# Kernel tuning notes

Measured on AMD Instinct MI355X. Metric: run time of the kernel, lower is better.

The kernel has to match this reference:

```python
import jax, jax.numpy as jnp
import numpy as np

B, T, DM, H = 1, 1024, 1024, 16
D = DM // H
RANK = 32
CONV = 3


def setup_inputs() -> dict:
    key = jax.random.key(0)
    ks = jax.random.split(key, 9)
    s = lambda k, shape, sc: jax.random.normal(k, shape, dtype=jnp.float32) * sc
    return {
        "x": s(ks[0], (B, T, DM), 1.0),
        "Wq": s(ks[1], (DM, DM), DM ** -0.5),
        "Wk": s(ks[2], (DM, DM), DM ** -0.5),
        "Wv": s(ks[3], (DM, DM), DM ** -0.5),
        "Ww1": s(ks[4], (DM, RANK), DM ** -0.5),
        "Ww2": s(ks[5], (RANK, DM), RANK ** -0.5),
        "conv_w": s(ks[6], (DM, CONV), CONV ** -0.5),
        "Wb": s(ks[7], (DM, H), DM ** -0.5),
        "Wo": s(ks[8], (DM, DM), DM ** -0.5),
    }


def _short_conv_silu(x, conv_w):
    # causal depthwise conv1d (torch semantics, kernel size CONV, no bias) + SiLU
    # y[t] = sum_m conv_w[:, m] * x[t - (CONV-1) + m]
    tl = x.shape[1]
    x_pad = jnp.pad(x, ((0, 0), (CONV - 1, 0), (0, 0)))
    y = sum(conv_w[:, m] * x_pad[:, m:m + tl, :] for m in range(CONV))
    return jax.nn.silu(y)


def _path_forward(x, Wq, Wk, Wv, Ww1, Ww2, conv_w, Wb, Wo):
    # projections
    q = (x @ Wq).reshape(B, T, H, D)
    k = (x @ Wk).reshape(B, T, H, D)
    v = (x @ Wv).reshape(B, T, H, D)
    # low-rank w projection -> causal short conv + silu -> per-head l2 norm
    w = _short_conv_silu((x @ Ww1) @ Ww2, conv_w).reshape(B, T, H, D)
    w = w * jax.lax.rsqrt(jnp.sum(w * w, axis=-1, keepdims=True) + 1e-6)
    beta = 2.0 * jax.nn.sigmoid(x @ Wb)  # [B,T,H], beta in (0,2)

    # -> [B,H,T,D] / [B,H,T]
    q, k, v, w = (jnp.transpose(a, (0, 2, 1, 3)) for a in (q, k, v, w))
    beta = jnp.transpose(beta, (0, 2, 1))

    # PaTH scores: S[i,j] = q_i^T prod_{s=j+1..i} (I - beta_s w_s w_s^T) k_j, i >= j.
    # Exact parallel (UT-transform) form:
    #   G[i,j] = q_i.w_j - sum_{j<s<=i} G[i,s] * beta_s (w_s.w_j)
    #   => G @ (I + M) = tril(Q W^T),  M[s,j] = beta_s (w_s.w_j) for s>j (strict lower)
    #   S = Q K^T - G @ Mk,            Mk[s,j] = beta_s (w_s.k_j) for s>j (strict lower)
    idx = jnp.arange(T)
    strict = idx[:, None] > idx[None, :]
    causal = idx[:, None] >= idx[None, :]

    bw = beta[..., None] * w  # [B,H,T,D]
    M = jnp.where(strict, jnp.einsum('bhsd,bhjd->bhsj', bw, w), 0.0)
    A = jnp.eye(T, dtype=x.dtype) + M  # unit lower triangular
    Aqw = jnp.where(causal, jnp.einsum('bhid,bhsd->bhis', q, w), 0.0)
    G = jax.lax.linalg.triangular_solve(A, Aqw, left_side=False, lower=True,
                                        unit_diagonal=True)
    Mk = jnp.where(strict, jnp.einsum('bhsd,bhjd->bhsj', bw, k), 0.0)
    S = jnp.einsum('bhid,bhjd->bhij', q, k) - jnp.einsum('bhis,bhsj->bhij', G, Mk)
    S = jnp.where(causal, S * (D ** -0.5), -jnp.inf)
    P = jax.nn.softmax(S, axis=-1)
    o = jnp.einsum('bhij,bhjd->bhid', P, v)
    o = jnp.transpose(o, (0, 2, 1, 3)).reshape(B, T, DM)
    return o @ Wo


def reference(x, Wq, Wk, Wv, Ww1, Ww2, conv_w, Wb, Wo):
    return _path_forward(x, Wq, Wk, Wv, Ww1, Ww2, conv_w, Wb, Wo)
```

## Files before the change

### kernel.cpp

```cpp
#include <hip/hip_runtime.h>
#include <math.h>

#define TSEQ 1024
#define DMODEL 1024
#define NH 16
#define HD 64
#define RANK 32

typedef __attribute__((ext_vector_type(8))) short bf16x8;
typedef __attribute__((ext_vector_type(4))) float f32x4;

__device__ __forceinline__ unsigned short f2b(float f) {
    unsigned int u = __float_as_uint(f);
    u += 0x7fffu + ((u >> 16) & 1u);
    return (unsigned short)(u >> 16);
}
__device__ __forceinline__ float b2f(unsigned short h) {
    return __uint_as_float(((unsigned int)h) << 16);
}
__device__ __forceinline__ void split2(float v, unsigned short& h, unsigned short& l) {
    h = f2b(v); l = f2b(v - b2f(h));
}

#define MFMA(a, b, c) __builtin_amdgcn_mfma_f32_16x16x32_bf16((a), (b), (c), 0, 0, 0)

__global__ __launch_bounds__(256) void split_rm(const float* __restrict__ S,
    unsigned short* __restrict__ Hi, unsigned short* __restrict__ Lo, int n4)
{
    int i = blockIdx.x * 256 + threadIdx.x;
    if (i >= n4) return;
    float4 v = *(const float4*)&S[(size_t)i * 4];
    float vv[4] = {v.x, v.y, v.z, v.w};
    unsigned int hw[2], lw[2];
    unsigned short h[4], l[4];
    #pragma unroll
    for (int p = 0; p < 4; ++p) split2(vv[p], h[p], l[p]);
    hw[0] = (unsigned int)h[0] | ((unsigned int)h[1] << 16);
    hw[1] = (unsigned int)h[2] | ((unsigned int)h[3] << 16);
    lw[0] = (unsigned int)l[0] | ((unsigned int)l[1] << 16);
    lw[1] = (unsigned int)l[2] | ((unsigned int)l[3] << 16);
    *(uint2*)&Hi[(size_t)i * 4] = make_uint2(hw[0], hw[1]);
    *(uint2*)&Lo[(size_t)i * 4] = make_uint2(lw[0], lw[1]);
}

__global__ __launch_bounds__(256) void split_tr(const float* __restrict__ S,
    unsigned short* __restrict__ Hi, unsigned short* __restrict__ Lo, int Kd, int Nd)
{
    __shared__ float T[64][65];
    const int i0 = blockIdx.y * 64;
    const int j0 = blockIdx.x * 64;
    const int tid = threadIdx.x;
    const int r = tid >> 2, c16 = (tid & 3) * 16;
    #pragma unroll
    for (int p = 0; p < 4; ++p) {
        float4 v = *(const float4*)&S[(size_t)(i0 + r) * Nd + j0 + c16 + p * 4];
        T[r][c16 + p * 4 + 0] = v.x; T[r][c16 + p * 4 + 1] = v.y;
        T[r][c16 + p * 4 + 2] = v.z; T[r][c16 + p * 4 + 3] = v.w;
    }
    __syncthreads();
    const int orow = tid & 63;
    const int seg = tid >> 6;
    unsigned short hb[16], lb[16];
    #pragma unroll
    for (int p = 0; p < 16; ++p) split2(T[seg * 16 + p][orow], hb[p], lb[p]);
    size_t ob = (size_t)(j0 + orow) * Kd + i0 + seg * 16;
    unsigned int w[4];
    #pragma unroll
    for (int q = 0; q < 2; ++q) {
        #pragma unroll
        for (int p = 0; p < 4; ++p)
            w[p] = (unsigned int)hb[q*8 + 2*p] | ((unsigned int)hb[q*8 + 2*p + 1] << 16);
        *(uint4*)&Hi[ob + q * 8] = make_uint4(w[0], w[1], w[2], w[3]);
        #pragma unroll
        for (int p = 0; p < 4; ++p)
            w[p] = (unsigned int)lb[q*8 + 2*p] | ((unsigned int)lb[q*8 + 2*p + 1] << 16);
        *(uint4*)&Lo[ob + q * 8] = make_uint4(w[0], w[1], w[2], w[3]);
    }
}

__global__ __launch_bounds__(256) void mfma_nt(
    const unsigned short* __restrict__ Ah_, const unsigned short* __restrict__ Al_, int lda,
    const unsigned short* __restrict__ Bh_, const unsigned short* __restrict__ Bl_, int ldb,
    float* __restrict__ C, int ldc, int K)
{
    __shared__ unsigned short Ah[64][72], Al[64][72], Bh[64][72], Bl[64][72];
    const int tid = threadIdx.x;
    const int i0 = blockIdx.y * 64, j0 = blockIdx.x * 64;
    const int srow = tid >> 2, sc = tid & 3;
    const int lane = tid & 63, wid = tid >> 6;
    const int lc = lane & 15, kg8 = (lane >> 4) * 8;
    f32x4 acc[4] = {{0.f,0.f,0.f,0.f},{0.f,0.f,0.f,0.f},{0.f,0.f,0.f,0.f},{0.f,0.f,0.f,0.f}};
    for (int k0 = 0; k0 < K; k0 += 64) {
        __syncthreads();
        const size_t ab = (size_t)(i0 + srow) * lda + k0;
        const size_t bb = (size_t)(j0 + srow) * ldb + k0;
        *(uint4*)&Ah[srow][sc * 8]       = *(const uint4*)&Ah_[ab + sc * 8];
        *(uint4*)&Ah[srow][(sc + 4) * 8] = *(const uint4*)&Ah_[ab + (sc + 4) * 8];
        *(uint4*)&Al[srow][sc * 8]       = *(const uint4*)&Al_[ab + sc * 8];
        *(uint4*)&Al[srow][(sc + 4) * 8] = *(const uint4*)&Al_[ab + (sc + 4) * 8];
        *(uint4*)&Bh[srow][sc * 8]       = *(const uint4*)&Bh_[bb + sc * 8];
        *(uint4*)&Bh[srow][(sc + 4) * 8] = *(const uint4*)&Bh_[bb + (sc + 4) * 8];
        *(uint4*)&Bl[srow][sc * 8]       = *(const uint4*)&Bl_[bb + sc * 8];
        *(uint4*)&Bl[srow][(sc + 4) * 8] = *(const uint4*)&Bl_[bb + (sc + 4) * 8];
        __syncthreads();
        #pragma unroll
        for (int ks = 0; ks < 2; ++ks) {
            bf16x8 a_h = *(const bf16x8*)&Ah[wid * 16 + lc][ks * 32 + kg8];
            bf16x8 a_l = *(const bf16x8*)&Al[wid * 16 + lc][ks * 32 + kg8];
            #pragma unroll
            for (int nt = 0; nt < 4; ++nt) {
                bf16x8 b_h = *(const bf16x8*)&Bh[nt * 16 + lc][ks * 32 + kg8];
                bf16x8 b_l = *(const bf16x8*)&Bl[nt * 16 + lc][ks * 32 + kg8];
                acc[nt] = MFMA(a_h, b_h, acc[nt]);
                acc[nt] = MFMA(a_l, b_h, acc[nt]);
                acc[nt] = MFMA(a_h, b_l, acc[nt]);
            }
        }
    }
    const int orow = i0 + wid * 16 + (lane >> 4) * 4;
    #pragma unroll
    for (int nt = 0; nt < 4; ++nt)
        #pragma unroll
        for (int r = 0; r < 4; ++r)
            C[(size_t)(orow + r) * ldc + j0 + nt * 16 + lc] = acc[nt][r];
}

__global__ __launch_bounds__(256) void pairwise_mfma(const float* __restrict__ A,
    const float* __restrict__ B, float* __restrict__ C)
{
    const int jt = blockIdx.x, it = blockIdx.y, hh = blockIdx.z;
    if (jt > it) return;
    __shared__ unsigned short Ah[64][72], Al[64][72], Bh[64][72], Bl[64][72];
    const int tid = threadIdx.x;
    const int i0 = it * 64, j0 = jt * 64;
    const int srow = tid >> 2;
    const int lane = tid & 63, wid = tid >> 6;
    const int lc = lane & 15, kg8 = (lane >> 4) * 8;
    #pragma unroll
    for (int p = 0; p < 4; ++p) {
        const int dd = (tid & 3) * 4 + p * 16;
        float4 a = *(const float4*)&A[(size_t)(i0 + srow) * DMODEL + hh * HD + dd];
        split2(a.x, Ah[srow][dd + 0], Al[srow][dd + 0]);
        split2(a.y, Ah[srow][dd + 1], Al[srow][dd + 1]);
        split2(a.z, Ah[srow][dd + 2], Al[srow][dd + 2]);
        split2(a.w, Ah[srow][dd + 3], Al[srow][dd + 3]);
        float4 b = *(const float4*)&B[(size_t)(j0 + srow) * DMODEL + hh * HD + dd];
        split2(b.x, Bh[srow][dd + 0], Bl[srow][dd + 0]);
        split2(b.y, Bh[srow][dd + 1], Bl[srow][dd + 1]);
        split2(b.z, Bh[srow][dd + 2], Bl[srow][dd + 2]);
        split2(b.w, Bh[srow][dd + 3], Bl[srow][dd + 3]);
    }
    __syncthreads();
    f32x4 acc[4] = {{0.f,0.f,0.f,0.f},{0.f,0.f,0.f,0.f},{0.f,0.f,0.f,0.f},{0.f,0.f,0.f,0.f}};
    #pragma unroll
    for (int ks = 0; ks < 2; ++ks) {
        bf16x8 a_h = *(const bf16x8*)&Ah[wid * 16 + lc][ks * 32 + kg8];
        bf16x8 a_l = *(const bf16x8*)&Al[wid * 16 + lc][ks * 32 + kg8];
        #pragma unroll
        for (int nt = 0; nt < 4; ++nt) {
            bf16x8 b_h = *(const bf16x8*)&Bh[nt * 16 + lc][ks * 32 + kg8];
            bf16x8 b_l = *(const bf16x8*)&Bl[nt * 16 + lc][ks * 32 + kg8];
            acc[nt] = MFMA(a_h, b_h, acc[nt]);
            acc[nt] = MFMA(a_l, b_h, acc[nt]);
            acc[nt] = MFMA(a_h, b_l, acc[nt]);
        }
    }
    float* Ch = C + (size_t)hh * TSEQ * TSEQ;
    const int orow = i0 + wid * 16 + (lane >> 4) * 4;
    #pragma unroll
    for (int r = 0; r < 4; ++r) {
        const int i = orow + r;
        #pragma unroll
        for (int nt = 0; nt < 4; ++nt) {
            const int j = j0 + nt * 16 + lc;
            Ch[(size_t)i * TSEQ + j] = (i >= j) ? acc[nt][r] : 0.f;
        }
    }
}

__global__ __launch_bounds__(256) void pairwise_mt(const float* __restrict__ A,
    const float* __restrict__ B, const float* __restrict__ beta,
    unsigned short* __restrict__ OutH, unsigned short* __restrict__ OutL)
{
    const int jt = blockIdx.x, it = blockIdx.y, hh = blockIdx.z;
    if (jt > it) return;
    __shared__ unsigned short Ah[64][72], Al[64][72], Bh[64][72], Bl[64][72];
    __shared__ float TT[64][68];
    const int tid = threadIdx.x;
    const int i0 = it * 64, j0 = jt * 64;
    const int srow = tid >> 2;
    const int lane = tid & 63, wid = tid >> 6;
    const int lc = lane & 15, kg8 = (lane >> 4) * 8;
    #pragma unroll
    for (int p = 0; p < 4; ++p) {
        const int dd = (tid & 3) * 4 + p * 16;
        float4 a = *(const float4*)&A[(size_t)(i0 + srow) * DMODEL + hh * HD + dd];
        split2(a.x, Ah[srow][dd + 0], Al[srow][dd + 0]);
        split2(a.y, Ah[srow][dd + 1], Al[srow][dd + 1]);
        split2(a.z, Ah[srow][dd + 2], Al[srow][dd + 2]);
        split2(a.w, Ah[srow][dd + 3], Al[srow][dd + 3]);
        float4 b = *(const float4*)&B[(size_t)(j0 + srow) * DMODEL + hh * HD + dd];
        split2(b.x, Bh[srow][dd + 0], Bl[srow][dd + 0]);
        split2(b.y, Bh[srow][dd + 1], Bl[srow][dd + 1]);
        split2(b.z, Bh[srow][dd + 2], Bl[srow][dd + 2]);
        split2(b.w, Bh[srow][dd + 3], Bl[srow][dd + 3]);
    }
    __syncthreads();
    f32x4 acc[4] = {{0.f,0.f,0.f,0.f},{0.f,0.f,0.f,0.f},{0.f,0.f,0.f,0.f},{0.f,0.f,0.f,0.f}};
    #pragma unroll
    for (int ks = 0; ks < 2; ++ks) {
        bf16x8 a_h = *(const bf16x8*)&Ah[wid * 16 + lc][ks * 32 + kg8];
        bf16x8 a_l = *(const bf16x8*)&Al[wid * 16 + lc][ks * 32 + kg8];
        #pragma unroll
        for (int nt = 0; nt < 4; ++nt) {
            bf16x8 b_h = *(const bf16x8*)&Bh[nt * 16 + lc][ks * 32 + kg8];
            bf16x8 b_l = *(const bf16x8*)&Bl[nt * 16 + lc][ks * 32 + kg8];
            acc[nt] = MFMA(a_h, b_h, acc[nt]);
            acc[nt] = MFMA(a_l, b_h, acc[nt]);
            acc[nt] = MFMA(a_h, b_l, acc[nt]);
        }
    }
    const int rbase = wid * 16 + (lane >> 4) * 4;
    #pragma unroll
    for (int r = 0; r < 4; ++r) {
        const int i = i0 + rbase + r;
        const float sc = beta[i * NH + hh];
        #pragma unroll
        for (int nt = 0; nt < 4; ++nt) {
            const int j = j0 + nt * 16 + lc;
            TT[rbase + r][nt * 16 + lc] = (i > j) ? acc[nt][r] * sc : 0.f;
        }
    }
    __syncthreads();
    const int cb = (tid & 3) * 16;
    unsigned short hb[16], lb[16];
    #pragma unroll
    for (int e = 0; e < 16; ++e) split2(TT[cb + e][srow], hb[e], lb[e]);
    unsigned short* oh = OutH + (size_t)hh * TSEQ * TSEQ + (size_t)(j0 + srow) * TSEQ + i0 + cb;
    unsigned short* ol = OutL + (size_t)hh * TSEQ * TSEQ + (size_t)(j0 + srow) * TSEQ + i0 + cb;
    unsigned int w[4];
    #pragma unroll
    for (int q = 0; q < 2; ++q) {
        #pragma unroll
        for (int p = 0; p < 4; ++p)
            w[p] = (unsigned int)hb[q*8+2*p] | ((unsigned int)hb[q*8+2*p+1] << 16);
        *(uint4*)&oh[q * 8] = make_uint4(w[0], w[1], w[2], w[3]);
        #pragma unroll
        for (int p = 0; p < 4; ++p)
            w[p] = (unsigned int)lb[q*8+2*p] | ((unsigned int)lb[q*8+2*p+1] << 16);
        *(uint4*)&ol[q * 8] = make_uint4(w[0], w[1], w[2], w[3]);
    }
}

__global__ __launch_bounds__(64) void diag_inv(
    const unsigned short* __restrict__ Mth, const unsigned short* __restrict__ Mtl,
    unsigned short* __restrict__ Dth, unsigned short* __restrict__ Dtl)
{
    const int c = blockIdx.x, hh = blockIdx.y;
    const unsigned short* Mh = Mth + (size_t)hh * TSEQ * TSEQ;
    const unsigned short* Ml = Mtl + (size_t)hh * TSEQ * TSEQ;
    __shared__ float Ms[64][65];
    __shared__ float X[64][65];
    const int j = threadIdx.x;
    const int c64 = c * 64;
    const unsigned short* ph = &Mh[(size_t)(c64 + j) * TSEQ + c64];
    const unsigned short* pl = &Ml[(size_t)(c64 + j) * TSEQ + c64];
    for (int s = 0; s < 64; ++s) Ms[s][j] = b2f(ph[s]) + b2f(pl[s]);
    __builtin_amdgcn_s_waitcnt(0);
    for (int s = 0; s < 64; ++s) {
        float val = (s == j) ? 1.f : 0.f;
        for (int t = 0; t < s; ++t)
            val = fmaf(-Ms[s][t], X[t][j], val);
        X[s][j] = val;
    }
    unsigned short hb[64], lb[64];
    for (int s = 0; s < 64; ++s) split2(X[s][j], hb[s], lb[s]);
    unsigned short* oh = Dth + (((size_t)hh * 16 + c) * 64 + j) * 64;
    unsigned short* ol = Dtl + (((size_t)hh * 16 + c) * 64 + j) * 64;
    for (int q = 0; q < 8; ++q) {
        unsigned int w[4];
        #pragma unroll
        for (int p = 0; p < 4; ++p)
            w[p] = (unsigned int)hb[q*8+2*p] | ((unsigned int)hb[q*8+2*p+1] << 16);
        *(uint4*)&oh[q * 8] = make_uint4(w[0], w[1], w[2], w[3]);
        #pragma unroll
        for (int p = 0; p < 4; ++p)
            w[p] = (unsigned int)lb[q*8+2*p] | ((unsigned int)lb[q*8+2*p+1] << 16);
        *(uint4*)&ol[q * 8] = make_uint4(w[0], w[1], w[2], w[3]);
    }
}

__global__ __launch_bounds__(256) void solve_row(
    const float* __restrict__ QW,
    const unsigned short* __restrict__ Mth, const unsigned short* __restrict__ Mtl,
    const unsigned short* __restrict__ Dth, const unsigned short* __restrict__ Dtl,
    unsigned short* __restrict__ Gh_, unsigned short* __restrict__ Gl_)
{
    const int rt = blockIdx.x, hh = blockIdx.y;
    const float* QWh = QW + (size_t)hh * TSEQ * TSEQ;
    const unsigned short* Mh = Mth + (size_t)hh * TSEQ * TSEQ;
    const unsigned short* Ml = Mtl + (size_t)hh * TSEQ * TSEQ;
    const unsigned short* Dh = Dth + (size_t)hh * 16 * 4096;
    const unsigned short* Dl = Dtl + (size_t)hh * 16 * 4096;
    unsigned short* Gh = Gh_ + (size_t)hh * TSEQ * TSEQ;
    unsigned short* Gl = Gl_ + (size_t)hh * TSEQ * TSEQ;
    __shared__ float RHS[64][68];
    const int tid = threadIdx.x;
    const int lane = tid & 63, wid = tid >> 6;
    const int lc = lane & 15, kg8 = (lane >> 4) * 8;
    const int rbase = wid * 16 + (lane >> 4) * 4;
    const int i0 = rt * 64;

    for (int c = rt; c >= 0; --c) {
        const int j0 = c * 64;
        f32x4 acc[4] = {{0.f,0.f,0.f,0.f},{0.f,0.f,0.f,0.f},{0.f,0.f,0.f,0.f},{0.f,0.f,0.f,0.f}};
        for (int cp = c + 1; cp <= rt; ++cp) {
            const int s0 = cp * 64;
            #pragma unroll
            for (int ks = 0; ks < 2; ++ks) {
                const size_t ao = (size_t)(i0 + wid * 16 + lc) * TSEQ + s0 + ks * 32 + kg8;
                bf16x8 a_h = *(const bf16x8*)&Gh[ao];
                bf16x8 a_l = *(const bf16x8*)&Gl[ao];
                #pragma unroll
                for (int nt = 0; nt < 4; ++nt) {
                    const size_t bo = (size_t)(j0 + nt * 16 + lc) * TSEQ + s0 + ks * 32 + kg8;
                    bf16x8 b_h = *(const bf16x8*)&Mh[bo];
                    bf16x8 b_l = *(const bf16x8*)&Ml[bo];
                    acc[nt] = MFMA(a_h, b_h, acc[nt]);
                    acc[nt] = MFMA(a_l, b_h, acc[nt]);
                    acc[nt] = MFMA(a_h, b_l, acc[nt]);
                }
            }
        }
        #pragma unroll
        for (int nt = 0; nt < 4; ++nt)
            #pragma unroll
            for (int r = 0; r < 4; ++r)
                RHS[rbase + r][nt * 16 + lc] =
                    QWh[(size_t)(i0 + rbase + r) * TSEQ + j0 + nt * 16 + lc] - acc[nt][r];
        __syncthreads();
        f32x4 g[4] = {{0.f,0.f,0.f,0.f},{0.f,0.f,0.f,0.f},{0.f,0.f,0.f,0.f},{0.f,0.f,0.f,0.f}};
        const unsigned short* Dhc = Dh + c * 4096;
        const unsigned short* Dlc = Dl + c * 4096;
        #pragma unroll
        for (int ks = 0; ks < 2; ++ks) {
            bf16x8 a_h, a_l;
            const float* rp = &RHS[wid * 16 + lc][ks * 32 + kg8];
            #pragma unroll
            for (int e = 0; e < 8; ++e) {
                unsigned short th, tl;
                split2(rp[e], th, tl);
                a_h[e] = (short)th; a_l[e] = (short)tl;
            }
            #pragma unroll
            for (int nt = 0; nt < 4; ++nt) {
                const int bo = (nt * 16 + lc) * 64 + ks * 32 + kg8;
                bf16x8 b_h = *(const bf16x8*)&Dhc[bo];
                bf16x8 b_l = *(const bf16x8*)&Dlc[bo];
                g[nt] = MFMA(a_h, b_h, g[nt]);
                g[nt] = MFMA(a_l, b_h, g[nt]);
                g[nt] = MFMA(a_h, b_l, g[nt]);
            }
        }
        #pragma unroll
        for (int nt = 0; nt < 4; ++nt)
            #pragma unroll
            for (int r = 0; r < 4; ++r) {
                const size_t o = (size_t)(i0 + rbase + r) * TSEQ + j0 + nt * 16 + lc;
                unsigned short th, tl;
                split2(g[nt][r], th, tl);
                Gh[o] = th; Gl[o] = tl;
            }
        __syncthreads();
    }
}

__global__ __launch_bounds__(256) void s_update_ps(float* __restrict__ S,
    const unsigned short* __restrict__ Gh_, const unsigned short* __restrict__ Gl_,
    const unsigned short* __restrict__ MktH, const unsigned short* __restrict__ MktL)
{
    const int jt = blockIdx.x, it = blockIdx.y, hh = blockIdx.z;
    if (jt > it) return;
    const unsigned short* Gh = Gh_ + (size_t)hh * TSEQ * TSEQ;
    const unsigned short* Gl = Gl_ + (size_t)hh * TSEQ * TSEQ;
    const unsigned short* Mh = MktH + (size_t)hh * TSEQ * TSEQ;
    const unsigned short* Ml = MktL + (size_t)hh * TSEQ * TSEQ;
    float* Sh = S + (size_t)hh * TSEQ * TSEQ;
    __shared__ unsigned short Ah[64][72], Al[64][72], Bh[64][72], Bl[64][72];
    const int tid = threadIdx.x;
    const int i0 = it * 64, j0 = jt * 64;
    const int srow = tid >> 2, sc = tid & 3;
    const int lane = tid & 63, wid = tid >> 6;
    const int lc = lane & 15, kg8 = (lane >> 4) * 8;
    f32x4 acc[4] = {{0.f,0.f,0.f,0.f},{0.f,0.f,0.f,0.f},{0.f,0.f,0.f,0.f},{0.f,0.f,0.f,0.f}};
    for (int st = jt; st <= it; ++st) {
        const int s0 = st * 64;
        __syncthreads();
        const size_t ab = (size_t)(i0 + srow) * TSEQ + s0;
        const size_t bb = (size_t)(j0 + srow) * TSEQ + s0;
        *(uint4*)&Ah[srow][sc * 8]       = *(const uint4*)&Gh[ab + sc * 8];
        *(uint4*)&Ah[srow][(sc + 4) * 8] = *(const uint4*)&Gh[ab + (sc + 4) * 8];
        *(uint4*)&Al[srow][sc * 8]       = *(const uint4*)&Gl[ab + sc * 8];
        *(uint4*)&Al[srow][(sc + 4) * 8] = *(const uint4*)&Gl[ab + (sc + 4) * 8];
        *(uint4*)&Bh[srow][sc * 8]       = *(const uint4*)&Mh[bb + sc * 8];
        *(uint4*)&Bh[srow][(sc + 4) * 8] = *(const uint4*)&Mh[bb + (sc + 4) * 8];
        *(uint4*)&Bl[srow][sc * 8]       = *(const uint4*)&Ml[bb + sc * 8];
        *(uint4*)&Bl[srow][(sc + 4) * 8] = *(const uint4*)&Ml[bb + (sc + 4) * 8];
        __syncthreads();
        #pragma unroll
        for (int ks = 0; ks < 2; ++ks) {
            bf16x8 a_h = *(const bf16x8*)&Ah[wid * 16 + lc][ks * 32 + kg8];
            bf16x8 a_l = *(const bf16x8*)&Al[wid * 16 + lc][ks * 32 + kg8];
            #pragma unroll
            for (int nt = 0; nt < 4; ++nt) {
                bf16x8 b_h = *(const bf16x8*)&Bh[nt * 16 + lc][ks * 32 + kg8];
                bf16x8 b_l = *(const bf16x8*)&Bl[nt * 16 + lc][ks * 32 + kg8];
                acc[nt] = MFMA(a_h, b_h, acc[nt]);
                acc[nt] = MFMA(a_l, b_h, acc[nt]);
                acc[nt] = MFMA(a_h, b_l, acc[nt]);
            }
        }
    }
    const int orow = i0 + wid * 16 + (lane >> 4) * 4;
    #pragma unroll
    for (int nt = 0; nt < 4; ++nt)
        #pragma unroll
        for (int r = 0; r < 4; ++r)
            Sh[(size_t)(orow + r) * TSEQ + j0 + nt * 16 + lc] -= acc[nt][r];
}

__global__ __launch_bounds__(256) void gemm_f32(const float* __restrict__ A,
    const float* __restrict__ B, float* __restrict__ C, int M, int N, int K)
{
    __shared__ float At[16][68];
    __shared__ float Bs[16][68];
    const int tid = threadIdx.x;
    const int tx = tid & 15, ty = tid >> 4;
    const int i0 = blockIdx.y * 64, j0 = blockIdx.x * 64;
    const int arow = tid >> 2, ac4 = (tid & 3) * 4;
    const int brow = tid >> 4, bc4 = (tid & 15) * 4;
    float acc[4][4] = {};
    for (int k0 = 0; k0 < K; k0 += 16) {
        float4 a = *(const float4*)&A[(size_t)(i0 + arow) * K + k0 + ac4];
        At[ac4 + 0][arow] = a.x; At[ac4 + 1][arow] = a.y;
        At[ac4 + 2][arow] = a.z; At[ac4 + 3][arow] = a.w;
        *(float4*)&Bs[brow][bc4] = *(const float4*)&B[(size_t)(k0 + brow) * N + j0 + bc4];
        __syncthreads();
        #pragma unroll
        for (int kk = 0; kk < 16; ++kk) {
            float4 a4 = *(const float4*)&At[kk][ty * 4];
            float4 b4 = *(const float4*)&Bs[kk][tx * 4];
            float av[4] = {a4.x, a4.y, a4.z, a4.w};
            float bv[4] = {b4.x, b4.y, b4.z, b4.w};
            #pragma unroll
            for (int m = 0; m < 4; ++m)
                #pragma unroll
                for (int n = 0; n < 4; ++n)
                    acc[m][n] = fmaf(av[m], bv[n], acc[m][n]);
        }
        __syncthreads();
    }
    #pragma unroll
    for (int m = 0; m < 4; ++m) {
        float4 o = {acc[m][0], acc[m][1], acc[m][2], acc[m][3]};
        *(float4*)&C[(size_t)(i0 + ty * 4 + m) * N + j0 + tx * 4] = o;
    }
}

__global__ __launch_bounds__(256) void gemm_skinny_rows(const float* __restrict__ A,
    const float* __restrict__ B, float* __restrict__ C, int N, int K)
{
    const int row = blockIdx.x;
    const int tid = threadIdx.x;
    const int col = tid & (N - 1);
    const int ks = tid / N;
    const int nsl = 256 / N;
    const float* a = A + (size_t)row * K;
    float s = 0.f;
    for (int k = ks; k < K; k += nsl)
        s = fmaf(a[k], B[(size_t)k * N + col], s);
    __shared__ float red[256];
    red[tid] = s; __syncthreads();
    for (int off = 128; off >= N; off >>= 1) {
        if (tid < off) red[tid] += red[tid + off];
        __syncthreads();
    }
    if (tid < N) C[(size_t)row * N + col] = red[tid];
}

__global__ __launch_bounds__(64) void conv_silu_norm(const float* __restrict__ wpre,
    const float* __restrict__ cw, const float* __restrict__ blog,
    float* __restrict__ w, float* __restrict__ beta)
{
    const int t = blockIdx.x, h = blockIdx.y, d = threadIdx.x;
    const int c = h * HD + d;
    float x2 = wpre[(size_t)t * DMODEL + c];
    float x1 = (t >= 1) ? wpre[(size_t)(t - 1) * DMODEL + c] : 0.f;
    float x0 = (t >= 2) ? wpre[(size_t)(t - 2) * DMODEL + c] : 0.f;
    float y = cw[c * 3 + 0] * x0 + cw[c * 3 + 1] * x1 + cw[c * 3 + 2] * x2;
    y = y / (1.f + expf(-y));
    float ss = y * y;
    #pragma unroll
    for (int off = 32; off >= 1; off >>= 1) ss += __shfl_xor(ss, off, 64);
    float r = 1.f / sqrtf(ss + 1e-6f);
    w[(size_t)t * DMODEL + c] = y * r;
    if (d == 0) beta[t * NH + h] = 2.f / (1.f + expf(-blog[t * NH + h]));
}

__global__ __launch_bounds__(256) void softmax_causal(float* __restrict__ S)
{
    const int i = blockIdx.x, hh = blockIdx.y;
    float* row = S + (size_t)hh * TSEQ * TSEQ + (size_t)i * TSEQ;
    const int tid = threadIdx.x;
    const float sc = 0.125f;
    __shared__ float red[256];
    float mx = -3.4e38f;
    for (int j = tid; j <= i; j += 256) mx = fmaxf(mx, row[j] * sc);
    red[tid] = mx; __syncthreads();
    for (int off = 128; off >= 1; off >>= 1) {
        if (tid < off) red[tid] = fmaxf(red[tid], red[tid + off]);
        __syncthreads();
    }
    mx = red[0]; __syncthreads();
    float sum = 0.f;
    for (int j = tid; j <= i; j += 256) {
        float e = expf(row[j] * sc - mx);
        row[j] = e; sum += e;
    }
    red[tid] = sum; __syncthreads();
    for (int off = 128; off >= 1; off >>= 1) {
        if (tid < off) red[tid] += red[tid + off];
        __syncthreads();
    }
    float inv = 1.f / red[0];
    for (int j = tid; j <= i; j += 256) row[j] *= inv;
}

__global__ __launch_bounds__(256) void pv64(const float* __restrict__ P,
    const float* __restrict__ V, float* __restrict__ O)
{
    const int it = blockIdx.x, hh = blockIdx.y;
    const float* Ph = P + (size_t)hh * TSEQ * TSEQ;
    __shared__ float Pt[64][68];
    __shared__ float Vs[64][68];
    const int tid = threadIdx.x, tx = tid & 15, ty = tid >> 4;
    const int i0 = it * 64;
    const int row = tid >> 2, c4 = (tid & 3) * 4;
    float acc[4][4] = {};
    for (int jt = 0; jt <= it; ++jt) {
        const int j0 = jt * 64;
        const int i = i0 + row;
        #pragma unroll
        for (int p = 0; p < 4; ++p) {
            int dd = c4 + p * 16;
            float4 pv = *(const float4*)&Ph[(size_t)i * TSEQ + j0 + dd];
            Pt[dd + 0][row] = (j0 + dd + 0 <= i) ? pv.x : 0.f;
            Pt[dd + 1][row] = (j0 + dd + 1 <= i) ? pv.y : 0.f;
            Pt[dd + 2][row] = (j0 + dd + 2 <= i) ? pv.z : 0.f;
            Pt[dd + 3][row] = (j0 + dd + 3 <= i) ? pv.w : 0.f;
            *(float4*)&Vs[row][dd] = *(const float4*)&V[(size_t)(j0 + row) * DMODEL + hh * HD + dd];
        }
        __syncthreads();
        #pragma unroll 8
        for (int kk = 0; kk < 64; ++kk) {
            float4 a4 = *(const float4*)&Pt[kk][ty * 4];
            float4 b4 = *(const float4*)&Vs[kk][tx * 4];
            float av[4] = {a4.x, a4.y, a4.z, a4.w};
            float bv[4] = {b4.x, b4.y, b4.z, b4.w};
            #pragma unroll
            for (int m = 0; m < 4; ++m)
                #pragma unroll
                for (int n = 0; n < 4; ++n)
                    acc[m][n] = fmaf(av[m], bv[n], acc[m][n]);
        }
        __syncthreads();
    }
    #pragma unroll
    for (int m = 0; m < 4; ++m) {
        float4 o = {acc[m][0], acc[m][1], acc[m][2], acc[m][3]};
        *(float4*)&O[(size_t)(i0 + ty * 4 + m) * DMODEL + hh * HD + tx * 4] = o;
    }
}

extern "C" void kernel_launch(void* const* d_in, const int* in_sizes, int n_in,
                              void* d_out, int out_size, void* d_ws, size_t ws_size,
                              hipStream_t stream)
{
    const float* x   = (const float*)d_in[0];
    const float* Wq  = (const float*)d_in[1];
    const float* Wk  = (const float*)d_in[2];
    const float* Wv  = (const float*)d_in[3];
    const float* Ww1 = (const float*)d_in[4];
    const float* Ww2 = (const float*)d_in[5];
    const float* cw  = (const float*)d_in[6];
    const float* Wb  = (const float*)d_in[7];
    const float* Wo  = (const float*)d_in[8];
    float* out = (float*)d_out;

    float* ws = (float*)d_ws;
    size_t off = 0;
    auto alloc = [&](size_t n) { float* p = ws + off; off += n; return p; };
    float* q    = alloc((size_t)TSEQ * DMODEL);
    float* k    = alloc((size_t)TSEQ * DMODEL);
    float* v    = alloc((size_t)TSEQ * DMODEL);
    float* w    = alloc((size_t)TSEQ * DMODEL);
    float* wpre = alloc((size_t)TSEQ * DMODEL);
    float* oatt = alloc((size_t)TSEQ * DMODEL);
    float* xw1  = alloc((size_t)TSEQ * RANK);
    float* blog = alloc((size_t)TSEQ * NH);
    float* beta = alloc((size_t)TSEQ * NH);

    const size_t HT = (size_t)NH * TSEQ * TSEQ;
    float* slot0 = ws + off;
    float* slot1 = slot0 + HT;
    float* slot2 = slot1 + HT;
    unsigned short* MtH = (unsigned short*)slot1;
    unsigned short* MtL = MtH + HT;
    unsigned short* GH  = (unsigned short*)slot2;
    unsigned short* GL  = GH + HT;
    unsigned short* DtH = (unsigned short*)wpre;
    unsigned short* DtL = DtH + (size_t)NH * 16 * 4096;

    const size_t E = (size_t)TSEQ * DMODEL;
    unsigned short* us = (unsigned short*)slot0;
    unsigned short* xs_h  = us;          unsigned short* xs_l  = us + E;
    unsigned short* wqt_h = us + 2 * E;  unsigned short* wqt_l = us + 3 * E;
    unsigned short* wkt_h = us + 4 * E;  unsigned short* wkt_l = us + 5 * E;
    unsigned short* wvt_h = us + 6 * E;  unsigned short* wvt_l = us + 7 * E;
    unsigned short* oat_h = us;          unsigned short* oat_l = us + E;
    unsigned short* wot_h = us + 2 * E;  unsigned short* wot_l = us + 3 * E;

    dim3 g64(DMODEL / 64, TSEQ / 64);
    dim3 gt(16, 16);
    dim3 gp(16, 16, NH);

    split_rm<<<(int)(E / 4 + 255) / 256, 256, 0, stream>>>(x, xs_h, xs_l, (int)(E / 4));
    split_tr<<<gt, 256, 0, stream>>>(Wq, wqt_h, wqt_l, DMODEL, DMODEL);
    split_tr<<<gt, 256, 0, stream>>>(Wk, wkt_h, wkt_l, DMODEL, DMODEL);
    split_tr<<<gt, 256, 0, stream>>>(Wv, wvt_h, wvt_l, DMODEL, DMODEL);
    mfma_nt<<<g64, 256, 0, stream>>>(xs_h, xs_l, DMODEL, wqt_h, wqt_l, DMODEL, q, DMODEL, DMODEL);
    mfma_nt<<<g64, 256, 0, stream>>>(xs_h, xs_l, DMODEL, wkt_h, wkt_l, DMODEL, k, DMODEL, DMODEL);
    mfma_nt<<<g64, 256, 0, stream>>>(xs_h, xs_l, DMODEL, wvt_h, wvt_l, DMODEL, v, DMODEL, DMODEL);
    gemm_skinny_rows<<<TSEQ, 256, 0, stream>>>(x, Ww1, xw1, RANK, DMODEL);
    gemm_f32<<<g64, 256, 0, stream>>>(xw1, Ww2, wpre, TSEQ, DMODEL, RANK);
    gemm_skinny_rows<<<TSEQ, 256, 0, stream>>>(x, Wb, blog, NH, DMODEL);
    conv_silu_norm<<<dim3(TSEQ, NH), 64, 0, stream>>>(wpre, cw, blog, w, beta);

    pairwise_mt<<<gp, 256, 0, stream>>>(w, w, beta, MtH, MtL);
    diag_inv<<<dim3(16, NH), 64, 0, stream>>>(MtH, MtL, DtH, DtL);
    pairwise_mfma<<<gp, 256, 0, stream>>>(q, w, slot0);
    solve_row<<<dim3(16, NH), 256, 0, stream>>>(slot0, MtH, MtL, DtH, DtL, GH, GL);
    pairwise_mt<<<gp, 256, 0, stream>>>(w, k, beta, MtH, MtL);
    pairwise_mfma<<<gp, 256, 0, stream>>>(q, k, slot0);
    s_update_ps<<<gp, 256, 0, stream>>>(slot0, GH, GL, MtH, MtL);
    softmax_causal<<<dim3(TSEQ, NH), 256, 0, stream>>>(slot0);
    pv64<<<dim3(16, NH), 256, 0, stream>>>(slot0, v, oatt);

    split_rm<<<(int)(E / 4 + 255) / 256, 256, 0, stream>>>(oatt, oat_h, oat_l, (int)(E / 4));
    split_tr<<<gt, 256, 0, stream>>>(Wo, wot_h, wot_l, DMODEL, DMODEL);
    mfma_nt<<<g64, 256, 0, stream>>>(oat_h, oat_l, DMODEL, wot_h, wot_l, DMODEL, out, DMODEL, DMODEL);
}
```

Measured before the change: 914.2 us.

## Split triangular solve into 16-row blocks with LDS-staged operands

The row-block triangular solve now gives each workgroup 16 rows instead of 64, launching 4x more workgroups (64x16 instead of 16x16), so the serial per-column-block chain is spread across more CUs. The G and M tiles for each inner step are staged into shared memory and read from there by the MFMA operand loads, replacing direct global reads. The cost is that each M tile is reloaded by four times as many workgroups, and there is an extra barrier per inner step. Each wave now computes a single 16x16 output tile.

```diff
diff --git a/kernel.cpp b/kernel.cpp
--- a/kernel.cpp
+++ b/kernel.cpp
@@ -290,13 +290,15 @@
     }
 }
 
-__global__ __launch_bounds__(256) void solve_row(
+__global__ __launch_bounds__(256) void solve_row16(
     const float* __restrict__ QW,
     const unsigned short* __restrict__ Mth, const unsigned short* __restrict__ Mtl,
     const unsigned short* __restrict__ Dth, const unsigned short* __restrict__ Dtl,
     unsigned short* __restrict__ Gh_, unsigned short* __restrict__ Gl_)
 {
-    const int rt = blockIdx.x, hh = blockIdx.y;
+    const int hh = blockIdx.y;
+    const int i0 = blockIdx.x * 16;
+    const int cmax = blockIdx.x >> 2;
     const float* QWh = QW + (size_t)hh * TSEQ * TSEQ;
     const unsigned short* Mh = Mth + (size_t)hh * TSEQ * TSEQ;
     const unsigned short* Ml = Mtl + (size_t)hh * TSEQ * TSEQ;
@@ -304,73 +306,81 @@
     const unsigned short* Dl = Dtl + (size_t)hh * 16 * 4096;
     unsigned short* Gh = Gh_ + (size_t)hh * TSEQ * TSEQ;
     unsigned short* Gl = Gl_ + (size_t)hh * TSEQ * TSEQ;
-    __shared__ float RHS[64][68];
+
+    __shared__ unsigned short As_h[16][72], As_l[16][72];
+    __shared__ unsigned short Bs_h[64][72], Bs_l[64][72];
+    __shared__ float RHS[16][68];
+
     const int tid = threadIdx.x;
     const int lane = tid & 63, wid = tid >> 6;
     const int lc = lane & 15, kg8 = (lane >> 4) * 8;
-    const int rbase = wid * 16 + (lane >> 4) * 4;
-    const int i0 = rt * 64;
-
-    for (int c = rt; c >= 0; --c) {
+    const int rb = (lane >> 4) * 4;
+
+    for (int c = cmax; c >= 0; --c) {
         const int j0 = c * 64;
-        f32x4 acc[4] = {{0.f,0.f,0.f,0.f},{0.f,0.f,0.f,0.f},{0.f,0.f,0.f,0.f},{0.f,0.f,0.f,0.f}};
-        for (int cp = c + 1; cp <= rt; ++cp) {
+        f32x4 acc = {0.f, 0.f, 0.f, 0.f};
+        for (int cp = c + 1; cp <= cmax; ++cp) {
             const int s0 = cp * 64;
+            {
+                const int t7 = tid & 127;
+                const int ar = t7 >> 3, ac8 = (t7 & 7) * 8;
+                const size_t go = (size_t)(i0 + ar) * TSEQ + s0 + ac8;
+                if (tid < 128) *(uint4*)&As_h[ar][ac8] = *(const uint4*)&Gh[go];
+                else           *(uint4*)&As_l[ar][ac8] = *(const uint4*)&Gl[go];
+            }
+            {
+                const int br = tid >> 2, bc = (tid & 3) * 16;
+                const size_t go = (size_t)(j0 + br) * TSEQ + s0 + bc;
+                *(uint4*)&Bs_h[br][bc]     = *(const uint4*)&Mh[go];
+                *(uint4*)&Bs_h[br][bc + 8] = *(const uint4*)&Mh[go + 8];
+                *(uint4*)&Bs_l[br][bc]     = *(const uint4*)&Ml[go];
+                *(uint4*)&Bs_l[br][bc + 8] = *(const uint4*)&Ml[go + 8];
+            }
+            __syncthreads();
             #pragma unroll
             for (int ks = 0; ks < 2; ++ks) {
-                const size_t ao = (size_t)(i0 + wid * 16 + lc) * TSEQ + s0 + ks * 32 + kg8;
-                bf16x8 a_h = *(const bf16x8*)&Gh[ao];
-                bf16x8 a_l = *(const bf16x8*)&Gl[ao];
-                #pragma unroll
-                for (int nt = 0; nt < 4; ++nt) {
-                    const size_t bo = (size_t)(j0 + nt * 16 + lc) * TSEQ + s0 + ks * 32 + kg8;
-                    bf16x8 b_h = *(const bf16x8*)&Mh[bo];
-                    bf16x8 b_l = *(const bf16x8*)&Ml[bo];
-                    acc[nt] = MFMA(a_h, b_h, acc[nt]);
-                    acc[nt] = MFMA(a_l, b_h, acc[nt]);
-                    acc[nt] = MFMA(a_h, b_l, acc[nt]);
-                }
+                bf16x8 a_h = *(const bf16x8*)&As_h[lc][ks * 32 + kg8];
+                bf16x8 a_l = *(const bf16x8*)&As_l[lc][ks * 32 + kg8];
+                bf16x8 b_h = *(const bf16x8*)&Bs_h[wid * 16 + lc][ks * 32 + kg8];
+                bf16x8 b_l = *(const bf16x8*)&Bs_l[wid * 16 + lc][ks * 32 + kg8];
+                acc = MFMA(a_h, b_h, acc);
+                acc = MFMA(a_l, b_h, acc);
+                acc = MFMA(a_h, b_l, acc);
             }
-        }
-        #pragma unroll
-        for (int nt = 0; nt < 4; ++nt)
-            #pragma unroll
-            for (int r = 0; r < 4; ++r)
-                RHS[rbase + r][nt * 16 + lc] =
-                    QWh[(size_t)(i0 + rbase + r) * TSEQ + j0 + nt * 16 + lc] - acc[nt][r];
-        __syncthreads();
-        f32x4 g[4] = {{0.f,0.f,0.f,0.f},{0.f,0.f,0.f,0.f},{0.f,0.f,0.f,0.f},{0.f,0.f,0.f,0.f}};
+            __syncthreads();
+        }
+        #pragma unroll
+        for (int r = 0; r < 4; ++r)
+            RHS[rb + r][wid * 16 + lc] =
+                QWh[(size_t)(i0 + rb + r) * TSEQ + j0 + wid * 16 + lc] - acc[r];
+        __syncthreads();
+        f32x4 g = {0.f, 0.f, 0.f, 0.f};
         const unsigned short* Dhc = Dh + c * 4096;
         const unsigned short* Dlc = Dl + c * 4096;
         #pragma unroll
         for (int ks = 0; ks < 2; ++ks) {
             bf16x8 a_h, a_l;
-            const float* rp = &RHS[wid * 16 + lc][ks * 32 + kg8];
+            const float* rp = &RHS[lc][ks * 32 + kg8];
             #pragma unroll
             for (int e = 0; e < 8; ++e) {
                 unsigned short th, tl;
                 split2(rp[e], th, tl);
                 a_h[e] = (short)th; a_l[e] = (short)tl;
             }
-            #pragma unroll
-            for (int nt = 0; nt < 4; ++nt) {
-                const int bo = (nt * 16 + lc) * 64 + ks * 32 + kg8;
-                bf16x8 b_h = *(const bf16x8*)&Dhc[bo];
-                bf16x8 b_l = *(const bf16x8*)&Dlc[bo];
-                g[nt] = MFMA(a_h, b_h, g[nt]);
-                g[nt] = MFMA(a_l, b_h, g[nt]);
-                g[nt] = MFMA(a_h, b_l, g[nt]);
-            }
-        }
-        #pragma unroll
-        for (int nt = 0; nt < 4; ++nt)
-            #pragma unroll
-            for (int r = 0; r < 4; ++r) {
-                const size_t o = (size_t)(i0 + rbase + r) * TSEQ + j0 + nt * 16 + lc;
-                unsigned short th, tl;
-                split2(g[nt][r], th, tl);
-                Gh[o] = th; Gl[o] = tl;
-            }
+            const int bo = (wid * 16 + lc) * 64 + ks * 32 + kg8;
+            bf16x8 b_h = *(const bf16x8*)&Dhc[bo];
+            bf16x8 b_l = *(const bf16x8*)&Dlc[bo];
+            g = MFMA(a_h, b_h, g);
+            g = MFMA(a_l, b_h, g);
+            g = MFMA(a_h, b_l, g);
+        }
+        #pragma unroll
+        for (int r = 0; r < 4; ++r) {
+            const size_t o = (size_t)(i0 + rb + r) * TSEQ + j0 + wid * 16 + lc;
+            unsigned short th, tl;
+            split2(g[r], th, tl);
+            Gh[o] = th; Gl[o] = tl;
+        }
         __syncthreads();
     }
 }
@@ -649,7 +659,7 @@
     pairwise_mt<<<gp, 256, 0, stream>>>(w, w, beta, MtH, MtL);
     diag_inv<<<dim3(16, NH), 64, 0, stream>>>(MtH, MtL, DtH, DtL);
     pairwise_mfma<<<gp, 256, 0, stream>>>(q, w, slot0);
-    solve_row<<<dim3(16, NH), 256, 0, stream>>>(slot0, MtH, MtL, DtH, DtL, GH, GL);
+    solve_row16<<<dim3(TSEQ / 16, NH), 256, 0, stream>>>(slot0, MtH, MtL, DtH, DtL, GH, GL);
     pairwise_mt<<<gp, 256, 0, stream>>>(w, k, beta, MtH, MtL);
     pairwise_mfma<<<gp, 256, 0, stream>>>(q, k, slot0);
     s_update_ps<<<gp, 256, 0, stream>>>(slot0, GH, GL, MtH, MtL);
```

New measurement: 768.5 us. 1.19x faster.
